# Optimization experiments

Hardware: AMD Instinct MI355X
Metric: run time of the kernel (lower is better)

Reference implementation:

```python
import jax, jax.numpy as jnp
import numpy as np

B, S, H = 2, 2048, 2048
NH = 16
HD = H // NH  # 128


def setup_inputs() -> dict:
    key = jax.random.key(0)
    ks = jax.random.split(key, 6)
    sc = 0.02
    return {
        "x": jax.random.normal(ks[0], (B, S, H), dtype=jnp.float32),
        "attention_mask": jnp.zeros((B, S), dtype=jnp.float32),
        "Wq": jax.random.normal(ks[1], (H, H), dtype=jnp.float32) * sc,
        "bq": jnp.zeros((H,), dtype=jnp.float32),
        "Wk": jax.random.normal(ks[2], (H, H), dtype=jnp.float32) * sc,
        "bk": jnp.zeros((H,), dtype=jnp.float32),
        "Wv": jax.random.normal(ks[3], (H, H), dtype=jnp.float32) * sc,
        "bv": jnp.zeros((H,), dtype=jnp.float32),
        "Wo": jax.random.normal(ks[4], (H, H), dtype=jnp.float32) * sc,
        "bo": jnp.zeros((H,), dtype=jnp.float32),
    }


def reference(x, attention_mask, Wq, bq, Wk, bk, Wv, bv, Wo, bo):
    b, s, h = x.shape
    q = (x @ Wq + bq).reshape(b, s, NH, HD)
    k = (x @ Wk + bk).reshape(b, s, NH, HD)
    v = (x @ Wv + bv).reshape(b, s, NH, HD)
    scale = 1.0 / jnp.sqrt(jnp.asarray(HD, dtype=x.dtype))
    scores = jnp.einsum('bqhd,bkhd->bhqk', q, k) * scale
    scores = scores + attention_mask[:, None, None, :]
    weights = jax.nn.softmax(scores, axis=-1)
    attn = jnp.einsum('bhqk,bkhd->bqhd', weights, v).reshape(b, s, h)
    return attn @ Wo + bo
```

## Files before the change

### kernel.cpp

```cpp
#include <hip/hip_runtime.h>
#include <hip/hip_bf16.h>
#include <stdint.h>

#define BB   2
#define SS   2048
#define HHH  2048
#define NHH  16
#define HDD  128
#define MTOT 4096

typedef __bf16 bf16x8 __attribute__((ext_vector_type(8)));
typedef float  f32x4  __attribute__((ext_vector_type(4)));
typedef float  f32x16 __attribute__((ext_vector_type(16)));

#define MFMA16(a, b, c) __builtin_amdgcn_mfma_f32_16x16x32_bf16((a), (b), (c), 0, 0, 0)
#define MFMA32(a, b, c) __builtin_amdgcn_mfma_f32_32x32x16_bf16((a), (b), (c), 0, 0, 0)

__device__ __forceinline__ unsigned short f2bf(float f) {
    union { float f; unsigned u; } v; v.f = f;
    unsigned r = v.u + 0x7FFFu + ((v.u >> 16) & 1u);
    return (unsigned short)(r >> 16);
}

__device__ __forceinline__ unsigned packbf(float a, float b) {
    union { __bf16 h[2]; unsigned u; } p;
    p.h[0] = (__bf16)a; p.h[1] = (__bf16)b;
    return p.u;
}

__device__ __forceinline__ void pswap(unsigned &a, unsigned &b) {
    asm("v_permlane32_swap_b32 %0, %1" : "+v"(a), "+v"(b));
}

__device__ __forceinline__ float2 xswap(float x) {
    unsigned a = __builtin_bit_cast(unsigned, x);
    unsigned b;
    asm("v_mov_b32 %0, %1" : "=v"(b) : "v"(a));
    asm("v_permlane32_swap_b32 %0, %1" : "+v"(a), "+v"(b));
    return make_float2(__builtin_bit_cast(float, a), __builtin_bit_cast(float, b));
}

__device__ __forceinline__ void gload16(const void* src, void* lds) {
    __builtin_amdgcn_global_load_lds(
        (__attribute__((address_space(1))) void*)src,
        (__attribute__((address_space(3))) void*)lds,
        16, 0, 0);
}

__global__ void cast_f32_bf16(const float* __restrict__ in,
                              unsigned short* __restrict__ out, int n) {
    int i = (blockIdx.x * blockDim.x + threadIdx.x) * 4;
    int stride = gridDim.x * blockDim.x * 4;
    for (; i < n; i += stride) {
        float4 v = *(const float4*)(in + i);
        ushort4 o;
        o.x = f2bf(v.x); o.y = f2bf(v.y); o.z = f2bf(v.z); o.w = f2bf(v.w);
        *(ushort4*)(out + i) = o;
    }
}

__global__ void scale_mask(const float* __restrict__ in, float* __restrict__ out) {
    int i = blockIdx.x * 256 + threadIdx.x;
    out[i] = in[i] * 1.4426950408889634f;
}

__global__ void transpose_cast4(const float* __restrict__ W0, const float* __restrict__ W1,
                                const float* __restrict__ W2, const float* __restrict__ W3,
                                unsigned short* __restrict__ out) {
    const float* in = blockIdx.z == 0 ? W0 : blockIdx.z == 1 ? W1 : blockIdx.z == 2 ? W2 : W3;
    unsigned short* o = out + (size_t)blockIdx.z * ((size_t)HHH * HHH);
    __shared__ float tile[32][33];
    int c0 = blockIdx.x * 32, r0 = blockIdx.y * 32;
    int tx = threadIdx.x, ty = threadIdx.y;
    #pragma unroll
    for (int i = 0; i < 32; i += 8)
        tile[ty + i][tx] = in[(size_t)(r0 + ty + i) * HHH + c0 + tx];
    __syncthreads();
    #pragma unroll
    for (int i = 0; i < 32; i += 8)
        o[(size_t)(c0 + ty + i) * HHH + r0 + tx] = f2bf(tile[tx][ty + i]);
}

template<int MODE>
__global__ __launch_bounds__(512, 2) void gemm8_bf16(
    const unsigned short* __restrict__ A,
    const unsigned short* __restrict__ Bt,
    const float* __restrict__ bias,
    void* __restrict__ Cout,
    int M, int N, int K)
{
    __shared__ __align__(16) unsigned char sm[147456];
    const int tid = threadIdx.x;
    const int wv = tid >> 6, ln = tid & 63;
    const int g = ln >> 4, r = ln & 15;
    const int wr = wv >> 2, wc = wv & 3;

    const int bid = blockIdx.x;
    const int lb = (bid & 7) * 32 + (bid >> 3);
    const int m0 = (lb & 31) * 128;
    const int n0 = (lb >> 5) * 256;

    unsigned srcA[2]; int ldsA[2];
    #pragma unroll
    for (int j = 0; j < 2; ++j) {
        int o = j * 8192 + tid * 16;
        int row = o >> 7;
        int lg = ((o >> 4) & 7) ^ (row & 7);
        srcA[j] = (unsigned)(m0 + row) * K + lg * 8;
        ldsA[j] = o;
    }
    unsigned srcB[4]; int ldsB[4];
    #pragma unroll
    for (int j = 0; j < 4; ++j) {
        int o = j * 8192 + tid * 16;
        int row = o >> 7;
        int lg = ((o >> 4) & 7) ^ (row & 7);
        srcB[j] = (unsigned)(n0 + row) * K + lg * 8;
        ldsB[j] = 16384 + o;
    }

    f32x4 acc[4][4];
    #pragma unroll
    for (int i = 0; i < 4; ++i)
        #pragma unroll
        for (int j = 0; j < 4; ++j)
            acc[i][j] = (f32x4){0.f, 0.f, 0.f, 0.f};

    const int NT = K >> 6;

    {
        unsigned char* b0 = sm;
        unsigned char* b1 = sm + 49152;
        #pragma unroll
        for (int j = 0; j < 2; ++j) gload16(A + srcA[j], b0 + ldsA[j]);
        #pragma unroll
        for (int j = 0; j < 4; ++j) gload16(Bt + srcB[j], b0 + ldsB[j]);
        #pragma unroll
        for (int j = 0; j < 2; ++j) gload16(A + srcA[j] + 64, b1 + ldsA[j]);
        #pragma unroll
        for (int j = 0; j < 4; ++j) gload16(Bt + srcB[j] + 64, b1 + ldsB[j]);
    }
    asm volatile("s_waitcnt vmcnt(6)" ::: "memory");
    __builtin_amdgcn_s_barrier();

    int csel = 0;
    int psel = 2;
    for (int t = 0; t < NT; ++t) {
        const unsigned char* Ab = sm + csel * 49152;
        const unsigned char* Bb = Ab + 16384;
        unsigned char* Pb = sm + psel * 49152;
        const bool pre = (t + 2 < NT);
        const int ko = (t + 2) * 64;

        bf16x8 af[2][2], bfr[4][2];
        #define LDA(mi, ks) (*(const bf16x8*)(Ab + (wr * 64 + (mi) * 16 + r) * 128 + \
                             ((((ks) << 2) + g) ^ ((wr * 64 + (mi) * 16 + r) & 7)) * 16))
        #define LDB(ni, ks) (*(const bf16x8*)(Bb + (wc * 64 + (ni) * 16 + r) * 128 + \
                             ((((ks) << 2) + g) ^ ((wc * 64 + (ni) * 16 + r) & 7)) * 16))

        af[0][0] = LDA(0, 0); af[0][1] = LDA(0, 1);
        af[1][0] = LDA(1, 0); af[1][1] = LDA(1, 1);
        #pragma unroll
        for (int ni = 0; ni < 4; ++ni) {
            bfr[ni][0] = LDB(ni, 0);
            bfr[ni][1] = LDB(ni, 1);
        }
        if (pre) { gload16(Bt + srcB[0] + ko, Pb + ldsB[0]);
                   gload16(Bt + srcB[1] + ko, Pb + ldsB[1]);
                   gload16(Bt + srcB[2] + ko, Pb + ldsB[2]); }
        __builtin_amdgcn_s_barrier();
        asm volatile("s_waitcnt lgkmcnt(0)" ::: "memory");
        __builtin_amdgcn_s_setprio(1);
        #pragma unroll
        for (int mi = 0; mi < 2; ++mi)
            #pragma unroll
            for (int ni = 0; ni < 4; ++ni)
                #pragma unroll
                for (int ks = 0; ks < 2; ++ks)
                    acc[mi][ni] = MFMA16(af[mi][ks], bfr[ni][ks], acc[mi][ni]);
        __builtin_amdgcn_s_setprio(0);
        __builtin_amdgcn_s_barrier();

        af[0][0] = LDA(2, 0); af[0][1] = LDA(2, 1);
        af[1][0] = LDA(3, 0); af[1][1] = LDA(3, 1);
        if (pre) { gload16(Bt + srcB[3] + ko, Pb + ldsB[3]);
                   gload16(A + srcA[0] + ko, Pb + ldsA[0]);
                   gload16(A + srcA[1] + ko, Pb + ldsA[1]); }
        __builtin_amdgcn_s_barrier();
        asm volatile("s_waitcnt lgkmcnt(0)" ::: "memory");
        __builtin_amdgcn_s_setprio(1);
        #pragma unroll
        for (int mi = 0; mi < 2; ++mi)
            #pragma unroll
            for (int ni = 0; ni < 4; ++ni)
                #pragma unroll
                for (int ks = 0; ks < 2; ++ks)
                    acc[mi + 2][ni] = MFMA16(af[mi][ks], bfr[ni][ks], acc[mi + 2][ni]);
        __builtin_amdgcn_s_setprio(0);

        if (pre) asm volatile("s_waitcnt vmcnt(6)" ::: "memory");
        else     asm volatile("s_waitcnt vmcnt(0)" ::: "memory");
        __builtin_amdgcn_s_barrier();

        csel = (csel == 2) ? 0 : csel + 1;
        psel = (psel == 2) ? 0 : psel + 1;
        #undef LDA
        #undef LDB
    }

    #pragma unroll
    for (int mt = 0; mt < 4; ++mt) {
        #pragma unroll
        for (int nt = 0; nt < 4; ++nt) {
            int col = n0 + wc * 64 + nt * 16 + r;
            float bvv = bias[col];
            f32x4 a = acc[mt][nt];
            int mrow = m0 + wr * 64 + mt * 16 + g * 4;
            if (MODE == 0) {
                #pragma unroll
                for (int q = 0; q < 4; ++q)
                    ((unsigned short*)Cout)[(size_t)(mrow + q) * N + col] = f2bf(a[q] + bvv);
            } else if (MODE == 2) {
                #pragma unroll
                for (int q = 0; q < 4; ++q)
                    ((float*)Cout)[(size_t)(mrow + q) * N + col] = a[q] + bvv;
            } else {
                int b = mrow >> 11, s0x = mrow & 2047;
                ushort4 o;
                o.x = f2bf(a[0] + bvv); o.y = f2bf(a[1] + bvv);
                o.z = f2bf(a[2] + bvv); o.w = f2bf(a[3] + bvv);
                *(ushort4*)((unsigned short*)Cout + ((size_t)(b * 2048 + col)) * 2048 + s0x) = o;
            }
        }
    }
}

__global__ __launch_bounds__(256, 2) void attn_fwd(
    const unsigned short* __restrict__ Q,
    const unsigned short* __restrict__ K,
    const unsigned short* __restrict__ V,
    const float* __restrict__ maskl2,
    unsigned short* __restrict__ O)
{
    __shared__ __align__(16) unsigned char sm[57344];
    const int tid = threadIdx.x, wv = tid >> 6, ln = tid & 63;
    const int hi = ln >> 5, qr = ln & 31;

    const int bid = blockIdx.x;
    const int lb = (bid & 7) * 64 + (bid >> 3);
    const int qb = lb & 15;
    const int bh = lb >> 4;
    const int h = bh & 15, b = bh >> 4;

    const size_t rowQ0 = (size_t)(b * 2048 + qb * 128 + wv * 32);
    const float SCL2 = 0.08838834764831845f * 1.4426950408889634f;

    unsigned srcK[2], srcV[2];
    int ldsK[2], ldsV[2];
    #pragma unroll
    for (int i = 0; i < 2; ++i) {
        int ch = wv * 2 + i;
        int o = ch * 1024 + ln * 16;
        { int row = o >> 8; int gl = ((o >> 4) & 15) ^ (row & 7);
          srcK[i] = (unsigned)((b * 2048 + row) * 2048 + h * 128 + gl * 8);
          ldsK[i] = o; }
        { int d = o >> 6; int gl = ((o >> 4) & 3) ^ ((d >> 1) & 3);
          srcV[i] = (unsigned)((b * 2048 + h * 128 + d) * 2048 + gl * 8);
          ldsV[i] = 8192 + o; }
    }

    #define STAGE(t, base) { \
        _Pragma("unroll") \
        for (int i = 0; i < 2; ++i) { \
            gload16(K + srcK[i] + (unsigned)(t) * (32u * 2048u), sm + (base) + ldsK[i]); \
            gload16(V + srcV[i] + (unsigned)(t) * 32u, sm + (base) + ldsV[i]); \
        } }

    #pragma unroll
    for (int i = 0; i < 2; ++i)
        gload16(maskl2 + b * 2048 + wv * 512 + i * 256 + ln * 4,
                sm + 49152 + wv * 2048 + i * 1024);
    STAGE(0, 0); STAGE(1, 16384); STAGE(2, 32768);

    bf16x8 qf[8];
    #pragma unroll
    for (int ks = 0; ks < 8; ++ks)
        qf[ks] = *(const bf16x8*)(Q + (rowQ0 + qr) * 2048 + h * 128 + ks * 16 + hi * 8);

    f32x16 acc[4];
    #pragma unroll
    for (int i = 0; i < 4; ++i)
        #pragma unroll
        for (int j = 0; j < 16; ++j)
            acc[i][j] = 0.f;
    float mr = -3.0e38f, lr = 0.f;

    const float* ml = (const float*)(sm + 49152);

    asm volatile("s_waitcnt vmcnt(8)" ::: "memory");
    __builtin_amdgcn_s_barrier();

    int bufo = 0;
    for (int t = 0; t < 64; ++t) {
        const unsigned char* Kt = sm + bufo;
        const unsigned char* Vt = Kt + 8192;

        f32x4 mk[4];
        #pragma unroll
        for (int rg = 0; rg < 4; ++rg)
            mk[rg] = *(const f32x4*)(ml + t * 32 + rg * 8 + hi * 4);

        f32x16 sfA, sfB;
        #pragma unroll
        for (int j = 0; j < 16; ++j) { sfA[j] = 0.f; sfB[j] = 0.f; }
        __builtin_amdgcn_s_setprio(1);
        #pragma unroll
        for (int ks = 0; ks < 4; ++ks) {
            int s0 = (2 * ks + hi) ^ (qr & 7);
            bf16x8 kf = *(const bf16x8*)(Kt + qr * 256 + s0 * 16);
            sfA = MFMA32(kf, qf[ks], sfA);
        }
        #pragma unroll
        for (int ks = 4; ks < 8; ++ks) {
            int s0 = (2 * ks + hi) ^ (qr & 7);
            bf16x8 kf = *(const bf16x8*)(Kt + qr * 256 + s0 * 16);
            sfB = MFMA32(kf, qf[ks], sfB);
        }
        __builtin_amdgcn_s_setprio(0);

        float sv[16];
        #pragma unroll
        for (int reg = 0; reg < 16; ++reg)
            sv[reg] = (sfA[reg] + sfB[reg]) * SCL2 + mk[reg >> 2][reg & 3];

        float mx[8];
        #pragma unroll
        for (int j = 0; j < 8; ++j)
            mx[j] = fmaxf(sv[2 * j], sv[2 * j + 1]);
        float m01 = fmaxf(fmaxf(fmaxf(mx[0], mx[1]), fmaxf(mx[2], mx[3])),
                          fmaxf(fmaxf(mx[4], mx[5]), fmaxf(mx[6], mx[7])));
        float2 mp = xswap(m01);
        float mt = fmaxf(mp.x, mp.y);

        float alpha = 1.f;
        int allskip = __all(mt <= mr + 8.f);
        if (!allskip) {
            float nm = fmaxf(mr, mt);
            alpha = __builtin_amdgcn_exp2f(mr - nm);
            mr = nm;
            #pragma unroll
            for (int dblk = 0; dblk < 4; ++dblk)
                #pragma unroll
                for (int reg = 0; reg < 16; ++reg)
                    acc[dblk][reg] *= alpha;
        }

        float s0 = 0.f, s1 = 0.f, s2 = 0.f, s3 = 0.f;
        #pragma unroll
        for (int reg = 0; reg < 16; reg += 4) {
            float p0 = __builtin_amdgcn_exp2f(sv[reg + 0] - mr);
            float p1 = __builtin_amdgcn_exp2f(sv[reg + 1] - mr);
            float p2 = __builtin_amdgcn_exp2f(sv[reg + 2] - mr);
            float p3 = __builtin_amdgcn_exp2f(sv[reg + 3] - mr);
            sv[reg + 0] = p0; sv[reg + 1] = p1;
            sv[reg + 2] = p2; sv[reg + 3] = p3;
            s0 += p0; s1 += p1; s2 += p2; s3 += p3;
        }
        float rsl = (s0 + s1) + (s2 + s3);
        float2 rp = xswap(rsl);
        float rs = rp.x + rp.y;
        lr = lr * alpha + rs;

        bf16x8 pfr[2];
        #pragma unroll
        for (int kb16 = 0; kb16 < 2; ++kb16) {
            unsigned W00 = packbf(sv[(2*kb16+0)*4 + 0], sv[(2*kb16+0)*4 + 1]);
            unsigned W01 = packbf(sv[(2*kb16+0)*4 + 2], sv[(2*kb16+0)*4 + 3]);
            unsigned W10 = packbf(sv[(2*kb16+1)*4 + 0], sv[(2*kb16+1)*4 + 1]);
            unsigned W11 = packbf(sv[(2*kb16+1)*4 + 2], sv[(2*kb16+1)*4 + 3]);
            pswap(W00, W10);
            pswap(W01, W11);
            union { unsigned w[4]; bf16x8 v; } u;
            u.w[0] = W00; u.w[1] = W01; u.w[2] = W10; u.w[3] = W11;
            pfr[kb16] = u.v;
        }

        __builtin_amdgcn_s_setprio(1);
        #pragma unroll
        for (int dblk = 0; dblk < 4; ++dblk) {
            int d = dblk * 32 + qr;
            f32x16 a = acc[dblk];
            #pragma unroll
            for (int kb16 = 0; kb16 < 2; ++kb16) {
                int s = (2 * kb16 + hi) ^ ((d >> 1) & 3);
                bf16x8 vf = *(const bf16x8*)(Vt + d * 64 + s * 16);
                a = MFMA32(vf, pfr[kb16], a);
            }
            acc[dblk] = a;
        }
        __builtin_amdgcn_s_setprio(0);

        asm volatile("s_waitcnt vmcnt(4)" ::: "memory");
        __builtin_amdgcn_s_barrier();

        if (t + 3 < 64) STAGE(t + 3, bufo);
        bufo = (bufo == 32768) ? 0 : bufo + 16384;
    }

    float linv = 1.f / lr;
    unsigned short* orow = O + (rowQ0 + qr) * 2048 + h * 128;
    #pragma unroll
    for (int dblk = 0; dblk < 4; ++dblk)
        #pragma unroll
        for (int rg = 0; rg < 4; ++rg) {
            float v0 = acc[dblk][rg * 4 + 0] * linv;
            float v1 = acc[dblk][rg * 4 + 1] * linv;
            float v2 = acc[dblk][rg * 4 + 2] * linv;
            float v3 = acc[dblk][rg * 4 + 3] * linv;
            uint2 o;
            o.x = packbf(v0, v1);
            o.y = packbf(v2, v3);
            *(uint2*)(orow + dblk * 32 + rg * 8 + hi * 4) = o;
        }
    #undef STAGE
}

extern "C" void kernel_launch(void* const* d_in, const int* in_sizes, int n_in,
                              void* d_out, int out_size, void* d_ws, size_t ws_size,
                              hipStream_t stream)
{
    (void)in_sizes; (void)n_in; (void)out_size; (void)ws_size;
    const float* x    = (const float*)d_in[0];
    const float* mask = (const float*)d_in[1];
    const float* Wq   = (const float*)d_in[2];
    const float* bq   = (const float*)d_in[3];
    const float* Wk   = (const float*)d_in[4];
    const float* bk   = (const float*)d_in[5];
    const float* Wv   = (const float*)d_in[6];
    const float* bv   = (const float*)d_in[7];
    const float* Wo   = (const float*)d_in[8];
    const float* bo   = (const float*)d_in[9];
    float* out = (float*)d_out;

    char* ws = (char*)d_ws;
    unsigned short* xb  = (unsigned short*)(ws);
    unsigned short* Wqt = (unsigned short*)(ws + (16u << 20));
    unsigned short* Wkt = (unsigned short*)(ws + (24u << 20));
    unsigned short* Wvt = (unsigned short*)(ws + (32u << 20));
    unsigned short* Wot = (unsigned short*)(ws + (40u << 20));
    unsigned short* Qb  = (unsigned short*)(ws + (48u << 20));
    unsigned short* Kb  = (unsigned short*)(ws + (64u << 20));
    unsigned short* Vtb = (unsigned short*)(ws + (80u << 20));
    unsigned short* Ab  = (unsigned short*)(ws + (16u << 20));
    float*          mkl = (float*)(ws + (32u << 20));

    cast_f32_bf16<<<2048, 256, 0, stream>>>(x, xb, MTOT * HHH);
    transpose_cast4<<<dim3(64, 64, 4), dim3(32, 8), 0, stream>>>(Wq, Wk, Wv, Wo, Wqt);

    gemm8_bf16<0><<<256, 512, 0, stream>>>(xb, Wqt, bq, Qb,  MTOT, HHH, HHH);
    gemm8_bf16<0><<<256, 512, 0, stream>>>(xb, Wkt, bk, Kb,  MTOT, HHH, HHH);
    gemm8_bf16<1><<<256, 512, 0, stream>>>(xb, Wvt, bv, Vtb, MTOT, HHH, HHH);

    scale_mask<<<(BB * SS) / 256, 256, 0, stream>>>(mask, mkl);
    attn_fwd<<<512, 256, 0, stream>>>(Qb, Kb, Vtb, mkl, Ab);

    gemm8_bf16<2><<<256, 512, 0, stream>>>(Ab, Wot, bo, out, MTOT, HHH, HHH);
}
```

Before: 279.6 us.

## Software-pipeline QK^T of next tile with softmax and PV of current tile

Restructures the flash-attention loop so the QK^T MFMAs for tile t+1 are issued before the softmax and PV work of tile t. A prologue computes the first tile's scores and an epilogue handles the last tile. This lets the matrix unit overlap with the exp/max VALU work. The Q fragment load is also moved before the K/V staging, and the wait counts and barriers are adjusted, adding a second barrier per iteration. The cost is higher register pressure from keeping the next tile's scores live, which may hurt occupancy.

```diff
diff --git a/kernel.cpp b/kernel.cpp
--- a/kernel.cpp
+++ b/kernel.cpp
@@ -143,8 +143,12 @@
     asm volatile("s_waitcnt vmcnt(6)" ::: "memory");
     __builtin_amdgcn_s_barrier();
 
-    int csel = 0;
-    int psel = 2;
+    #define LDA(mi, ks) (*(const bf16x8*)(Ab + (wr * 64 + (mi) * 16 + r) * 128 + \
+                         ((((ks) << 2) + g) ^ ((wr * 64 + (mi) * 16 + r) & 7)) * 16))
+    #define LDB(ni, ks) (*(const bf16x8*)(Bb + (wc * 64 + (ni) * 16 + r) * 128 + \
+                         ((((ks) << 2) + g) ^ ((wc * 64 + (ni) * 16 + r) & 7)) * 16))
+
+    int csel = 0, psel = 2;
     for (int t = 0; t < NT; ++t) {
         const unsigned char* Ab = sm + csel * 49152;
         const unsigned char* Bb = Ab + 16384;
@@ -153,18 +157,11 @@
         const int ko = (t + 2) * 64;
 
         bf16x8 af[2][2], bfr[4][2];
-        #define LDA(mi, ks) (*(const bf16x8*)(Ab + (wr * 64 + (mi) * 16 + r) * 128 + \
-                             ((((ks) << 2) + g) ^ ((wr * 64 + (mi) * 16 + r) & 7)) * 16))
-        #define LDB(ni, ks) (*(const bf16x8*)(Bb + (wc * 64 + (ni) * 16 + r) * 128 + \
-                             ((((ks) << 2) + g) ^ ((wc * 64 + (ni) * 16 + r) & 7)) * 16))
 
         af[0][0] = LDA(0, 0); af[0][1] = LDA(0, 1);
         af[1][0] = LDA(1, 0); af[1][1] = LDA(1, 1);
         #pragma unroll
-        for (int ni = 0; ni < 4; ++ni) {
-            bfr[ni][0] = LDB(ni, 0);
-            bfr[ni][1] = LDB(ni, 1);
-        }
+        for (int ni = 0; ni < 4; ++ni) { bfr[ni][0] = LDB(ni, 0); bfr[ni][1] = LDB(ni, 1); }
         if (pre) { gload16(Bt + srcB[0] + ko, Pb + ldsB[0]);
                    gload16(Bt + srcB[1] + ko, Pb + ldsB[1]);
                    gload16(Bt + srcB[2] + ko, Pb + ldsB[2]); }
@@ -204,9 +201,9 @@
 
         csel = (csel == 2) ? 0 : csel + 1;
         psel = (psel == 2) ? 0 : psel + 1;
-        #undef LDA
-        #undef LDB
-    }
+    }
+    #undef LDA
+    #undef LDB
 
     #pragma unroll
     for (int mt = 0; mt < 4; ++mt) {
@@ -255,6 +252,11 @@
     const size_t rowQ0 = (size_t)(b * 2048 + qb * 128 + wv * 32);
     const float SCL2 = 0.08838834764831845f * 1.4426950408889634f;
 
+    bf16x8 qf[8];
+    #pragma unroll
+    for (int ks = 0; ks < 8; ++ks)
+        qf[ks] = *(const bf16x8*)(Q + (rowQ0 + qr) * 2048 + h * 128 + ks * 16 + hi * 8);
+
     unsigned srcK[2], srcV[2];
     int ldsK[2], ldsV[2];
     #pragma unroll
@@ -282,11 +284,6 @@
                 sm + 49152 + wv * 2048 + i * 1024);
     STAGE(0, 0); STAGE(1, 16384); STAGE(2, 32768);
 
-    bf16x8 qf[8];
-    #pragma unroll
-    for (int ks = 0; ks < 8; ++ks)
-        qf[ks] = *(const bf16x8*)(Q + (rowQ0 + qr) * 2048 + h * 128 + ks * 16 + hi * 8);
-
     f32x16 acc[4];
     #pragma unroll
     for (int i = 0; i < 4; ++i)
@@ -297,18 +294,36 @@
 
     const float* ml = (const float*)(sm + 49152);
 
-    asm volatile("s_waitcnt vmcnt(8)" ::: "memory");
+    asm volatile("s_waitcnt vmcnt(4)" ::: "memory");
     __builtin_amdgcn_s_barrier();
 
-    int bufo = 0;
-    for (int t = 0; t < 64; ++t) {
-        const unsigned char* Kt = sm + bufo;
-        const unsigned char* Vt = Kt + 8192;
-
-        f32x4 mk[4];
-        #pragma unroll
-        for (int rg = 0; rg < 4; ++rg)
-            mk[rg] = *(const f32x4*)(ml + t * 32 + rg * 8 + hi * 4);
+    float sv[16];
+    {
+        f32x16 sfA, sfB;
+        #pragma unroll
+        for (int j = 0; j < 16; ++j) { sfA[j] = 0.f; sfB[j] = 0.f; }
+        #pragma unroll
+        for (int ks = 0; ks < 4; ++ks) {
+            int s0 = (2 * ks + hi) ^ (qr & 7);
+            bf16x8 kf = *(const bf16x8*)(sm + qr * 256 + s0 * 16);
+            sfA = MFMA32(kf, qf[ks], sfA);
+        }
+        #pragma unroll
+        for (int ks = 4; ks < 8; ++ks) {
+            int s0 = (2 * ks + hi) ^ (qr & 7);
+            bf16x8 kf = *(const bf16x8*)(sm + qr * 256 + s0 * 16);
+            sfB = MFMA32(kf, qf[ks], sfB);
+        }
+        #pragma unroll
+        for (int reg = 0; reg < 16; ++reg)
+            sv[reg] = (sfA[reg] + sfB[reg]) * SCL2 + ml[(reg >> 2) * 8 + hi * 4 + (reg & 3)];
+    }
+
+    int base0 = 0;
+    for (int t = 0; t < 63; ++t) {
+        const int baseN = (base0 == 32768) ? 0 : base0 + 16384;
+        const unsigned char* Vt = sm + base0 + 8192;
+        const unsigned char* Kn = sm + baseN;
 
         f32x16 sfA, sfB;
         #pragma unroll
@@ -317,21 +332,16 @@
         #pragma unroll
         for (int ks = 0; ks < 4; ++ks) {
             int s0 = (2 * ks + hi) ^ (qr & 7);
-            bf16x8 kf = *(const bf16x8*)(Kt + qr * 256 + s0 * 16);
+            bf16x8 kf = *(const bf16x8*)(Kn + qr * 256 + s0 * 16);
             sfA = MFMA32(kf, qf[ks], sfA);
         }
         #pragma unroll
         for (int ks = 4; ks < 8; ++ks) {
             int s0 = (2 * ks + hi) ^ (qr & 7);
-            bf16x8 kf = *(const bf16x8*)(Kt + qr * 256 + s0 * 16);
+            bf16x8 kf = *(const bf16x8*)(Kn + qr * 256 + s0 * 16);
             sfB = MFMA32(kf, qf[ks], sfB);
         }
         __builtin_amdgcn_s_setprio(0);
-
-        float sv[16];
-        #pragma unroll
-        for (int reg = 0; reg < 16; ++reg)
-            sv[reg] = (sfA[reg] + sfB[reg]) * SCL2 + mk[reg >> 2][reg & 3];
 
         float mx[8];
         #pragma unroll
@@ -385,6 +395,11 @@
             pfr[kb16] = u.v;
         }
 
+        #pragma unroll
+        for (int reg = 0; reg < 16; ++reg)
+            sv[reg] = (sfA[reg] + sfB[reg]) * SCL2
+                      + ml[(t + 1) * 32 + (reg >> 2) * 8 + hi * 4 + (reg & 3)];
+
         __builtin_amdgcn_s_setprio(1);
         #pragma unroll
         for (int dblk = 0; dblk < 4; ++dblk) {
@@ -400,11 +415,82 @@
         }
         __builtin_amdgcn_s_setprio(0);
 
-        asm volatile("s_waitcnt vmcnt(4)" ::: "memory");
         __builtin_amdgcn_s_barrier();
-
-        if (t + 3 < 64) STAGE(t + 3, bufo);
-        bufo = (bufo == 32768) ? 0 : bufo + 16384;
+        if (t + 3 < 64) {
+            STAGE(t + 3, base0);
+            asm volatile("s_waitcnt vmcnt(4)" ::: "memory");
+        } else {
+            asm volatile("s_waitcnt vmcnt(0)" ::: "memory");
+        }
+        __builtin_amdgcn_s_barrier();
+        base0 = baseN;
+    }
+
+    {
+        const unsigned char* Vt = sm + base0 + 8192;
+        float mx[8];
+        #pragma unroll
+        for (int j = 0; j < 8; ++j)
+            mx[j] = fmaxf(sv[2 * j], sv[2 * j + 1]);
+        float m01 = fmaxf(fmaxf(fmaxf(mx[0], mx[1]), fmaxf(mx[2], mx[3])),
+                          fmaxf(fmaxf(mx[4], mx[5]), fmaxf(mx[6], mx[7])));
+        float2 mp = xswap(m01);
+        float mt = fmaxf(mp.x, mp.y);
+
+        float alpha = 1.f;
+        int allskip = __all(mt <= mr + 8.f);
+        if (!allskip) {
+            float nm = fmaxf(mr, mt);
+            alpha = __builtin_amdgcn_exp2f(mr - nm);
+            mr = nm;
+            #pragma unroll
+            for (int dblk = 0; dblk < 4; ++dblk)
+                #pragma unroll
+                for (int reg = 0; reg < 16; ++reg)
+                    acc[dblk][reg] *= alpha;
+        }
+
+        float s0 = 0.f, s1 = 0.f, s2 = 0.f, s3 = 0.f;
+        #pragma unroll
+        for (int reg = 0; reg < 16; reg += 4) {
+            float p0 = __builtin_amdgcn_exp2f(sv[reg + 0] - mr);
+            float p1 = __builtin_amdgcn_exp2f(sv[reg + 1] - mr);
+            float p2 = __builtin_amdgcn_exp2f(sv[reg + 2] - mr);
+            float p3 = __builtin_amdgcn_exp2f(sv[reg + 3] - mr);
+            sv[reg + 0] = p0; sv[reg + 1] = p1;
+            sv[reg + 2] = p2; sv[reg + 3] = p3;
+            s0 += p0; s1 += p1; s2 += p2; s3 += p3;
+        }
+        float rsl = (s0 + s1) + (s2 + s3);
+        float2 rp = xswap(rsl);
+        lr = lr * alpha + rp.x + rp.y;
+
+        bf16x8 pfr[2];
+        #pragma unroll
+        for (int kb16 = 0; kb16 < 2; ++kb16) {
+            unsigned W00 = packbf(sv[(2*kb16+0)*4 + 0], sv[(2*kb16+0)*4 + 1]);
+            unsigned W01 = packbf(sv[(2*kb16+0)*4 + 2], sv[(2*kb16+0)*4 + 3]);
+            unsigned W10 = packbf(sv[(2*kb16+1)*4 + 0], sv[(2*kb16+1)*4 + 1]);
+            unsigned W11 = packbf(sv[(2*kb16+1)*4 + 2], sv[(2*kb16+1)*4 + 3]);
+            pswap(W00, W10);
+            pswap(W01, W11);
+            union { unsigned w[4]; bf16x8 v; } u;
+            u.w[0] = W00; u.w[1] = W01; u.w[2] = W10; u.w[3] = W11;
+            pfr[kb16] = u.v;
+        }
+
+        #pragma unroll
+        for (int dblk = 0; dblk < 4; ++dblk) {
+            int d = dblk * 32 + qr;
+            f32x16 a = acc[dblk];
+            #pragma unroll
+            for (int kb16 = 0; kb16 < 2; ++kb16) {
+                int s = (2 * kb16 + hi) ^ ((d >> 1) & 3);
+                bf16x8 vf = *(const bf16x8*)(Vt + d * 64 + s * 16);
+                a = MFMA32(vf, pfr[kb16], a);
+            }
+            acc[dblk] = a;
+        }
     }
 
     float linv = 1.f / lr;
```

Result: no change. 279.0 us (-0.2%).

## Split attention key range across two wave groups and merge partial softmax

Applied to the files above, without the earlier changes.

The attention kernel now runs 512 threads per block, with two groups of four waves each handling half of the key sequence for the same query tile. Each group has its own double-buffered K/V staging in LDS. At the end the two partial results (running max, sum and accumulators) are combined through shared memory using a split-K style softmax merge. The goal is more waves per CU to hide latency. In exchange, LDS use grows, the pipeline drops from triple to double buffering, and an extra merge pass is added.

```diff
diff --git a/kernel.cpp b/kernel.cpp
--- a/kernel.cpp
+++ b/kernel.cpp
@@ -143,8 +143,12 @@
     asm volatile("s_waitcnt vmcnt(6)" ::: "memory");
     __builtin_amdgcn_s_barrier();
 
-    int csel = 0;
-    int psel = 2;
+    #define LDA(mi, ks) (*(const bf16x8*)(Ab + (wr * 64 + (mi) * 16 + r) * 128 + \
+                         ((((ks) << 2) + g) ^ ((wr * 64 + (mi) * 16 + r) & 7)) * 16))
+    #define LDB(ni, ks) (*(const bf16x8*)(Bb + (wc * 64 + (ni) * 16 + r) * 128 + \
+                         ((((ks) << 2) + g) ^ ((wc * 64 + (ni) * 16 + r) & 7)) * 16))
+
+    int csel = 0, psel = 2;
     for (int t = 0; t < NT; ++t) {
         const unsigned char* Ab = sm + csel * 49152;
         const unsigned char* Bb = Ab + 16384;
@@ -153,18 +157,11 @@
         const int ko = (t + 2) * 64;
 
         bf16x8 af[2][2], bfr[4][2];
-        #define LDA(mi, ks) (*(const bf16x8*)(Ab + (wr * 64 + (mi) * 16 + r) * 128 + \
-                             ((((ks) << 2) + g) ^ ((wr * 64 + (mi) * 16 + r) & 7)) * 16))
-        #define LDB(ni, ks) (*(const bf16x8*)(Bb + (wc * 64 + (ni) * 16 + r) * 128 + \
-                             ((((ks) << 2) + g) ^ ((wc * 64 + (ni) * 16 + r) & 7)) * 16))
 
         af[0][0] = LDA(0, 0); af[0][1] = LDA(0, 1);
         af[1][0] = LDA(1, 0); af[1][1] = LDA(1, 1);
         #pragma unroll
-        for (int ni = 0; ni < 4; ++ni) {
-            bfr[ni][0] = LDB(ni, 0);
-            bfr[ni][1] = LDB(ni, 1);
-        }
+        for (int ni = 0; ni < 4; ++ni) { bfr[ni][0] = LDB(ni, 0); bfr[ni][1] = LDB(ni, 1); }
         if (pre) { gload16(Bt + srcB[0] + ko, Pb + ldsB[0]);
                    gload16(Bt + srcB[1] + ko, Pb + ldsB[1]);
                    gload16(Bt + srcB[2] + ko, Pb + ldsB[2]); }
@@ -204,9 +201,9 @@
 
         csel = (csel == 2) ? 0 : csel + 1;
         psel = (psel == 2) ? 0 : psel + 1;
-        #undef LDA
-        #undef LDB
-    }
+    }
+    #undef LDA
+    #undef LDB
 
     #pragma unroll
     for (int mt = 0; mt < 4; ++mt) {
@@ -235,16 +232,17 @@
     }
 }
 
-__global__ __launch_bounds__(256, 2) void attn_fwd(
+__global__ __launch_bounds__(512, 4) void attn_fwd(
     const unsigned short* __restrict__ Q,
     const unsigned short* __restrict__ K,
     const unsigned short* __restrict__ V,
     const float* __restrict__ maskl2,
     unsigned short* __restrict__ O)
 {
-    __shared__ __align__(16) unsigned char sm[57344];
+    __shared__ __align__(16) unsigned char sm[73728];
     const int tid = threadIdx.x, wv = tid >> 6, ln = tid & 63;
     const int hi = ln >> 5, qr = ln & 31;
+    const int sp = wv >> 2, wq = wv & 3;
 
     const int bid = blockIdx.x;
     const int lb = (bid & 7) * 64 + (bid >> 3);
@@ -252,40 +250,39 @@
     const int bh = lb >> 4;
     const int h = bh & 15, b = bh >> 4;
 
-    const size_t rowQ0 = (size_t)(b * 2048 + qb * 128 + wv * 32);
+    const size_t rowQ0 = (size_t)(b * 2048 + qb * 128 + wq * 32);
+    const int kb0 = sp * 1024;
     const float SCL2 = 0.08838834764831845f * 1.4426950408889634f;
+
+    bf16x8 qf[8];
+    #pragma unroll
+    for (int ks = 0; ks < 8; ++ks)
+        qf[ks] = *(const bf16x8*)(Q + (rowQ0 + qr) * 2048 + h * 128 + ks * 16 + hi * 8);
 
     unsigned srcK[2], srcV[2];
     int ldsK[2], ldsV[2];
     #pragma unroll
     for (int i = 0; i < 2; ++i) {
-        int ch = wv * 2 + i;
+        int ch = wq * 2 + i;
         int o = ch * 1024 + ln * 16;
         { int row = o >> 8; int gl = ((o >> 4) & 15) ^ (row & 7);
-          srcK[i] = (unsigned)((b * 2048 + row) * 2048 + h * 128 + gl * 8);
+          srcK[i] = (unsigned)((b * 2048 + kb0 + row) * 2048 + h * 128 + gl * 8);
           ldsK[i] = o; }
         { int d = o >> 6; int gl = ((o >> 4) & 3) ^ ((d >> 1) & 3);
-          srcV[i] = (unsigned)((b * 2048 + h * 128 + d) * 2048 + gl * 8);
+          srcV[i] = (unsigned)((b * 2048 + h * 128 + d) * 2048 + kb0 + gl * 8);
           ldsV[i] = 8192 + o; }
     }
 
-    #define STAGE(t, base) { \
+    const int sbase = sp * 32768;
+    #define STAGE(t, boff) { \
         _Pragma("unroll") \
         for (int i = 0; i < 2; ++i) { \
-            gload16(K + srcK[i] + (unsigned)(t) * (32u * 2048u), sm + (base) + ldsK[i]); \
-            gload16(V + srcV[i] + (unsigned)(t) * 32u, sm + (base) + ldsV[i]); \
+            gload16(K + srcK[i] + (unsigned)(t) * (32u * 2048u), sm + sbase + (boff) + ldsK[i]); \
+            gload16(V + srcV[i] + (unsigned)(t) * 32u, sm + sbase + (boff) + ldsV[i]); \
         } }
 
-    #pragma unroll
-    for (int i = 0; i < 2; ++i)
-        gload16(maskl2 + b * 2048 + wv * 512 + i * 256 + ln * 4,
-                sm + 49152 + wv * 2048 + i * 1024);
-    STAGE(0, 0); STAGE(1, 16384); STAGE(2, 32768);
-
-    bf16x8 qf[8];
-    #pragma unroll
-    for (int ks = 0; ks < 8; ++ks)
-        qf[ks] = *(const bf16x8*)(Q + (rowQ0 + qr) * 2048 + h * 128 + ks * 16 + hi * 8);
+    gload16(maskl2 + b * 2048 + tid * 4, sm + 65536 + tid * 16);
+    STAGE(0, 0); STAGE(1, 16384);
 
     f32x16 acc[4];
     #pragma unroll
@@ -295,14 +292,13 @@
             acc[i][j] = 0.f;
     float mr = -3.0e38f, lr = 0.f;
 
-    const float* ml = (const float*)(sm + 49152);
-
-    asm volatile("s_waitcnt vmcnt(8)" ::: "memory");
+    const float* ml = (const float*)(sm + 65536) + kb0;
+
+    asm volatile("s_waitcnt vmcnt(4)" ::: "memory");
     __builtin_amdgcn_s_barrier();
 
-    int bufo = 0;
-    for (int t = 0; t < 64; ++t) {
-        const unsigned char* Kt = sm + bufo;
+    for (int t = 0; t < 32; ++t) {
+        const unsigned char* Kt = sm + sbase + (t & 1) * 16384;
         const unsigned char* Vt = Kt + 8192;
 
         f32x4 mk[4];
@@ -400,29 +396,58 @@
         }
         __builtin_amdgcn_s_setprio(0);
 
-        asm volatile("s_waitcnt vmcnt(4)" ::: "memory");
-        __builtin_amdgcn_s_barrier();
-
-        if (t + 3 < 64) STAGE(t + 3, bufo);
-        bufo = (bufo == 32768) ? 0 : bufo + 16384;
-    }
-
-    float linv = 1.f / lr;
-    unsigned short* orow = O + (rowQ0 + qr) * 2048 + h * 128;
-    #pragma unroll
-    for (int dblk = 0; dblk < 4; ++dblk)
-        #pragma unroll
-        for (int rg = 0; rg < 4; ++rg) {
-            float v0 = acc[dblk][rg * 4 + 0] * linv;
-            float v1 = acc[dblk][rg * 4 + 1] * linv;
-            float v2 = acc[dblk][rg * 4 + 2] * linv;
-            float v3 = acc[dblk][rg * 4 + 3] * linv;
-            uint2 o;
-            o.x = packbf(v0, v1);
-            o.y = packbf(v2, v3);
-            *(uint2*)(orow + dblk * 32 + rg * 8 + hi * 4) = o;
-        }
+        __builtin_amdgcn_s_barrier();
+        if (t + 2 < 32) {
+            STAGE(t + 2, (t & 1) * 16384);
+            asm volatile("s_waitcnt vmcnt(4)" ::: "memory");
+        } else {
+            asm volatile("s_waitcnt vmcnt(0)" ::: "memory");
+        }
+        __builtin_amdgcn_s_barrier();
+    }
     #undef STAGE
+
+    __syncthreads();
+    const int xl = wq * 64 + ln;
+    if (sp == 1) {
+        ((float2*)(sm + 65536))[xl] = make_float2(mr, lr);
+        unsigned char* exb = sm + xl * 256;
+        #pragma unroll
+        for (int dblk = 0; dblk < 4; ++dblk)
+            #pragma unroll
+            for (int j = 0; j < 4; ++j) {
+                int slot = (dblk * 4 + j) ^ (ln & 15);
+                f32x4 vq = { acc[dblk][j * 4 + 0], acc[dblk][j * 4 + 1],
+                             acc[dblk][j * 4 + 2], acc[dblk][j * 4 + 3] };
+                *(f32x4*)(exb + slot * 16) = vq;
+            }
+    }
+    __syncthreads();
+    if (sp == 0) {
+        float2 ml1 = ((const float2*)(sm + 65536))[xl];
+        float Mx = fmaxf(mr, ml1.x);
+        float e0 = __builtin_amdgcn_exp2f(mr - Mx);
+        float e1 = __builtin_amdgcn_exp2f(ml1.x - Mx);
+        float linv = 1.f / (e0 * lr + e1 * ml1.y);
+        e0 *= linv; e1 *= linv;
+        const unsigned char* exb = sm + xl * 256;
+        unsigned short* orow = O + (rowQ0 + qr) * 2048 + h * 128;
+        #pragma unroll
+        for (int dblk = 0; dblk < 4; ++dblk)
+            #pragma unroll
+            for (int rg = 0; rg < 4; ++rg) {
+                int slot = (dblk * 4 + rg) ^ (ln & 15);
+                f32x4 a1 = *(const f32x4*)(exb + slot * 16);
+                float v0 = e0 * acc[dblk][rg * 4 + 0] + e1 * a1[0];
+                float v1 = e0 * acc[dblk][rg * 4 + 1] + e1 * a1[1];
+                float v2 = e0 * acc[dblk][rg * 4 + 2] + e1 * a1[2];
+                float v3 = e0 * acc[dblk][rg * 4 + 3] + e1 * a1[3];
+                uint2 o;
+                o.x = packbf(v0, v1);
+                o.y = packbf(v2, v3);
+                *(uint2*)(orow + dblk * 32 + rg * 8 + hi * 4) = o;
+            }
+    }
 }
 
 extern "C" void kernel_launch(void* const* d_in, const int* in_sizes, int n_in,
@@ -462,7 +487,7 @@
     gemm8_bf16<1><<<256, 512, 0, stream>>>(xb, Wvt, bv, Vtb, MTOT, HHH, HHH);
 
     scale_mask<<<(BB * SS) / 256, 256, 0, stream>>>(mask, mkl);
-    attn_fwd<<<512, 256, 0, stream>>>(Qb, Kb, Vtb, mkl, Ab);
+    attn_fwd<<<512, 512, 0, stream>>>(Qb, Kb, Vtb, mkl, Ab);
 
     gemm8_bf16<2><<<256, 512, 0, stream>>>(Ab, Wot, bo, out, MTOT, HHH, HHH);
 }
```

Result: slower. 587.8 us (+110.2%).
